# Kernel optimization log

Measured on AMD Instinct MI355X. Metric: run time of the kernel, lower is better.

The kernel has to match this reference:

```python
import jax, jax.numpy as jnp
import numpy as np

N1, N2, K = 262144, 65536, 16   # dense points, coarse points, knn neighbors
CIN, COUT = 64, 64              # in_planes, out_planes
EPS = 1e-5


def bn(x, g, b, m, v):
    # eval-mode BatchNorm1d with learned affine and running stats
    return (x - m) * jax.lax.rsqrt(v + EPS) * g + b


def setup_inputs() -> dict:
    key = jax.random.key(0)
    ks = jax.random.split(key, 32)
    u = lambda k, *s: jax.random.normal(k, s, jnp.float32)
    lin = lambda k, o, i: jax.random.normal(k, (o, i), jnp.float32) / np.float32(np.sqrt(i))
    inp = dict(
        p1=u(ks[0], N1, 3), p2=u(ks[1], N2, 3),
        x1=u(ks[2], N1, COUT), x2=u(ks[3], N2, CIN),
        knn_idx=jax.random.randint(ks[4], (N2, K), 0, N1),
        # linear1: Linear(COUT,COUT) + BN + ReLU
        w1=lin(ks[5], COUT, COUT), b1=0.01 * u(ks[6], COUT),
        g1=jnp.ones(COUT), be1=jnp.zeros(COUT),
        m1=0.1 * u(ks[7], COUT), v1=jax.random.uniform(ks[8], (COUT,), minval=0.5, maxval=1.5),
        # linear2: Linear(CIN,COUT) + BN + ReLU
        w2=lin(ks[9], COUT, CIN), b2=0.01 * u(ks[10], COUT),
        g2=jnp.ones(COUT), be2=jnp.zeros(COUT),
        m2=0.1 * u(ks[11], COUT), v2=jax.random.uniform(ks[12], (COUT,), minval=0.5, maxval=1.5),
        # channel_shrinker: Linear(CIN+3,CIN) + BN + ReLU + Linear(CIN,1)
        ws1=lin(ks[13], CIN, CIN + 3), bs1=0.01 * u(ks[14], CIN),
        gs=jnp.ones(CIN), bes=jnp.zeros(CIN),
        ms=0.1 * u(ks[15], CIN), vs=jax.random.uniform(ks[16], (CIN,), minval=0.5, maxval=1.5),
        ws2=lin(ks[17], 1, CIN), bs2=0.01 * u(ks[18], 1),
    )
    return inp


def reference(p1, p2, x1, x2, knn_idx,
              w1, b1, g1, be1, m1, v1,
              w2, b2, g2, be2, m2, v2,
              ws1, bs1, gs, bes, ms, vs, ws2, bs2):
    idx = knn_idx.reshape(-1)                                   # [M] = [N2*K], indices into p1
    # relative position of each knn neighbor to its coarse query point
    p_r = p1[idx].reshape(N2, K, 3) - p2[:, None, :]            # [N2,K,3]
    x2k = jnp.concatenate(
        [p_r, jnp.broadcast_to(x2[:, None, :], (N2, K, CIN))], axis=-1
    ).reshape(N2 * K, CIN + 3)                                  # [M, CIN+3]
    # channel_shrinker MLP -> scalar logit per (coarse, neighbor) pair
    h = jax.nn.relu(bn(x2k @ ws1.T + bs1, gs, bes, ms, vs))     # [M, CIN]
    logit = (h @ ws2.T + bs2)[:, 0]                             # [M]
    # scatter_softmax over variable in-degree groups keyed by dense point idx
    gmax = jax.lax.stop_gradient(jax.ops.segment_max(logit, idx, num_segments=N1))
    e = jnp.exp(logit - gmax[idx])
    denom = jax.ops.segment_sum(e, idx, num_segments=N1)
    prob = e / denom[idx]                                       # [M]
    # linear2(x2), broadcast over K neighbors, weight, scatter-sum to dense points
    up_feat = jax.nn.relu(bn(x2 @ w2.T + b2, g2, be2, m2, v2))  # [N2, COUT]
    weighted = (up_feat[:, None, :] * prob.reshape(N2, K, 1)).reshape(N2 * K, COUT)
    up = jax.ops.segment_sum(weighted, idx, num_segments=N1)    # [N1, COUT]
    # skip branch: linear1(x1)
    y1 = jax.nn.relu(bn(x1 @ w1.T + b1, g1, be1, m1, v1))       # [N1, COUT]
    return y1 + up
```

## Files before the change

### kernel.cpp

```cpp
#include <hip/hip_runtime.h>

#define CN1 262144
#define CN2 65536
#define CK  16
#define CM  (CN2*CK)

typedef unsigned short u16;
typedef unsigned char  u8;
typedef unsigned int   u32;
typedef float f32x4 __attribute__((ext_vector_type(4)));

__device__ __forceinline__ float b2f(u16 h) {
    union { u32 u; float f; } v; v.u = ((u32)h) << 16; return v.f;
}
__device__ __forceinline__ u16 f2b(float f) {
    union { float f; u32 u; } v; v.f = f;
    u32 lsb = (v.u >> 16) & 1u;
    return (u16)((v.u + 0x7FFFu + lsb) >> 16);
}
__device__ __forceinline__ float u2f(u32 u) {
    union { u32 u; float f; } v; v.u = u; return v.f;
}
__device__ __forceinline__ u32 f2u(float f) {
    union { float f; u32 u; } v; v.f = f; return v.u;
}

#define W_POS   0
#define W_FT    256
#define W_AS    12544
#define W_BS    12608
#define W_WS2   12672
#define W_A2    12736
#define W_B2    12800
#define W_A1    12864
#define W_B1    12928
#define W_BS2   12992
#define W_MODE  13000
#define W_W1T   13056
#define W_W2T   17152
#define W_JP    21248

__device__ __forceinline__ float ldv(const void* p, size_t i, int bf) {
    return bf ? b2f(((const u16*)p)[i]) : ((const float*)p)[i];
}

#define FMA4(A, Wv) \
    (A).x = fmaf(xv_, (Wv).x, (A).x); (A).y = fmaf(xv_, (Wv).y, (A).y); \
    (A).z = fmaf(xv_, (Wv).z, (A).z); (A).w = fmaf(xv_, (Wv).w, (A).w);

#define DECL_ACC16 \
    f32x4 A0={0,0,0,0},A1={0,0,0,0},A2={0,0,0,0},A3={0,0,0,0}, \
          A4={0,0,0,0},A5={0,0,0,0},A6={0,0,0,0},A7={0,0,0,0}, \
          A8={0,0,0,0},A9={0,0,0,0},A10={0,0,0,0},A11={0,0,0,0}, \
          A12={0,0,0,0},A13={0,0,0,0},A14={0,0,0,0},A15={0,0,0,0};

#define WSTEP16(wt, ivar, xval) { \
    float xv_ = (xval); \
    const f32x4* wr_ = (const f32x4*)((wt) + ((size_t)(ivar) << 6)); \
    FMA4(A0, wr_[0])   FMA4(A1, wr_[1])   FMA4(A2, wr_[2])   FMA4(A3, wr_[3]) \
    FMA4(A4, wr_[4])   FMA4(A5, wr_[5])   FMA4(A6, wr_[6])   FMA4(A7, wr_[7]) \
    FMA4(A8, wr_[8])   FMA4(A9, wr_[9])   FMA4(A10,wr_[10])  FMA4(A11,wr_[11]) \
    FMA4(A12,wr_[12])  FMA4(A13,wr_[13])  FMA4(A14,wr_[14])  FMA4(A15,wr_[15]) }

#define GEMV64T(bf, xrow_f, xrow_u4, wt) \
    if (bf) { \
        const uint4* xu_ = (xrow_u4); \
        _Pragma("unroll 2") \
        for (int ii_ = 0; ii_ < 8; ++ii_) { \
            uint4 xc_ = xu_[ii_]; \
            WSTEP16(wt, ii_*8+0, b2f((u16)(xc_.x & 0xffffu))) \
            WSTEP16(wt, ii_*8+1, b2f((u16)(xc_.x >> 16))) \
            WSTEP16(wt, ii_*8+2, b2f((u16)(xc_.y & 0xffffu))) \
            WSTEP16(wt, ii_*8+3, b2f((u16)(xc_.y >> 16))) \
            WSTEP16(wt, ii_*8+4, b2f((u16)(xc_.z & 0xffffu))) \
            WSTEP16(wt, ii_*8+5, b2f((u16)(xc_.z >> 16))) \
            WSTEP16(wt, ii_*8+6, b2f((u16)(xc_.w & 0xffffu))) \
            WSTEP16(wt, ii_*8+7, b2f((u16)(xc_.w >> 16))) \
        } \
    } else { \
        const float4* xf_ = (xrow_f); \
        _Pragma("unroll 2") \
        for (int ii_ = 0; ii_ < 8; ++ii_) { \
            float4 xa_ = xf_[2*ii_], xb_ = xf_[2*ii_+1]; \
            WSTEP16(wt, ii_*8+0, xa_.x) WSTEP16(wt, ii_*8+1, xa_.y) \
            WSTEP16(wt, ii_*8+2, xa_.z) WSTEP16(wt, ii_*8+3, xa_.w) \
            WSTEP16(wt, ii_*8+4, xb_.x) WSTEP16(wt, ii_*8+5, xb_.y) \
            WSTEP16(wt, ii_*8+6, xb_.z) WSTEP16(wt, ii_*8+7, xb_.w) \
        } \
    }

#define DECL_ACC8 \
    f32x4 A0={0,0,0,0},A1={0,0,0,0},A2={0,0,0,0},A3={0,0,0,0}, \
          A4={0,0,0,0},A5={0,0,0,0},A6={0,0,0,0},A7={0,0,0,0};

#define WSTEP8(wtco, ivar, xval) { \
    float xv_ = (xval); \
    const f32x4* wr_ = (const f32x4*)((wtco) + ((size_t)(ivar) << 6)); \
    FMA4(A0, wr_[0])  FMA4(A1, wr_[1])  FMA4(A2, wr_[2])  FMA4(A3, wr_[3]) \
    FMA4(A4, wr_[4])  FMA4(A5, wr_[5])  FMA4(A6, wr_[6])  FMA4(A7, wr_[7]) }

#define GEMV32T(bf, xrow_f, xrow_u4, wtco) \
    if (bf) { \
        const uint4* xu_ = (xrow_u4); \
        _Pragma("unroll 2") \
        for (int ii_ = 0; ii_ < 8; ++ii_) { \
            uint4 xc_ = xu_[ii_]; \
            WSTEP8(wtco, ii_*8+0, b2f((u16)(xc_.x & 0xffffu))) \
            WSTEP8(wtco, ii_*8+1, b2f((u16)(xc_.x >> 16))) \
            WSTEP8(wtco, ii_*8+2, b2f((u16)(xc_.y & 0xffffu))) \
            WSTEP8(wtco, ii_*8+3, b2f((u16)(xc_.y >> 16))) \
            WSTEP8(wtco, ii_*8+4, b2f((u16)(xc_.z & 0xffffu))) \
            WSTEP8(wtco, ii_*8+5, b2f((u16)(xc_.z >> 16))) \
            WSTEP8(wtco, ii_*8+6, b2f((u16)(xc_.w & 0xffffu))) \
            WSTEP8(wtco, ii_*8+7, b2f((u16)(xc_.w >> 16))) \
        } \
    } else { \
        const float4* xf_ = (xrow_f); \
        _Pragma("unroll 2") \
        for (int ii_ = 0; ii_ < 8; ++ii_) { \
            float4 xa_ = xf_[2*ii_], xb_ = xf_[2*ii_+1]; \
            WSTEP8(wtco, ii_*8+0, xa_.x) WSTEP8(wtco, ii_*8+1, xa_.y) \
            WSTEP8(wtco, ii_*8+2, xa_.z) WSTEP8(wtco, ii_*8+3, xa_.w) \
            WSTEP8(wtco, ii_*8+4, xb_.x) WSTEP8(wtco, ii_*8+5, xb_.y) \
            WSTEP8(wtco, ii_*8+6, xb_.z) WSTEP8(wtco, ii_*8+7, xb_.w) \
        } \
    }

#define BNR1(A, av, bv) \
    (A).x = fmaxf(fmaf((A).x,(av).x,(bv).x),0.f); \
    (A).y = fmaxf(fmaf((A).y,(av).y,(bv).y),0.f); \
    (A).z = fmaxf(fmaf((A).z,(av).z,(bv).z),0.f); \
    (A).w = fmaxf(fmaf((A).w,(av).w,(bv).w),0.f);
#define BNR16(aBase, bBase) { \
    const f32x4* av_ = (const f32x4*)(aBase); \
    const f32x4* bv_ = (const f32x4*)(bBase); \
    BNR1(A0,av_[0],bv_[0])   BNR1(A1,av_[1],bv_[1]) \
    BNR1(A2,av_[2],bv_[2])   BNR1(A3,av_[3],bv_[3]) \
    BNR1(A4,av_[4],bv_[4])   BNR1(A5,av_[5],bv_[5]) \
    BNR1(A6,av_[6],bv_[6])   BNR1(A7,av_[7],bv_[7]) \
    BNR1(A8,av_[8],bv_[8])   BNR1(A9,av_[9],bv_[9]) \
    BNR1(A10,av_[10],bv_[10]) BNR1(A11,av_[11],bv_[11]) \
    BNR1(A12,av_[12],bv_[12]) BNR1(A13,av_[13],bv_[13]) \
    BNR1(A14,av_[14],bv_[14]) BNR1(A15,av_[15],bv_[15]) }
#define BNR8(aBase, bBase) { \
    const f32x4* av_ = (const f32x4*)(aBase); \
    const f32x4* bv_ = (const f32x4*)(bBase); \
    BNR1(A0,av_[0],bv_[0]) BNR1(A1,av_[1],bv_[1]) \
    BNR1(A2,av_[2],bv_[2]) BNR1(A3,av_[3],bv_[3]) \
    BNR1(A4,av_[4],bv_[4]) BNR1(A5,av_[5],bv_[5]) \
    BNR1(A6,av_[6],bv_[6]) BNR1(A7,av_[7],bv_[7]) }

#define UFQ(q, AL, AH) { uint4 u_ = ufr_[q]; \
    (AL).x = fmaf(pe_, b2f((u16)(u_.x & 0xffffu)), (AL).x); \
    (AL).y = fmaf(pe_, b2f((u16)(u_.x >> 16)),     (AL).y); \
    (AL).z = fmaf(pe_, b2f((u16)(u_.y & 0xffffu)), (AL).z); \
    (AL).w = fmaf(pe_, b2f((u16)(u_.y >> 16)),     (AL).w); \
    (AH).x = fmaf(pe_, b2f((u16)(u_.z & 0xffffu)), (AH).x); \
    (AH).y = fmaf(pe_, b2f((u16)(u_.z >> 16)),     (AH).y); \
    (AH).z = fmaf(pe_, b2f((u16)(u_.w & 0xffffu)), (AH).z); \
    (AH).w = fmaf(pe_, b2f((u16)(u_.w >> 16)),     (AH).w); }

#define STQ(q, AL, AH, dst) { uint4 o_; \
    o_.x = (u32)f2b((AL).x) | ((u32)f2b((AL).y) << 16); \
    o_.y = (u32)f2b((AL).z) | ((u32)f2b((AL).w) << 16); \
    o_.z = (u32)f2b((AH).x) | ((u32)f2b((AH).y) << 16); \
    o_.w = (u32)f2b((AH).z) | ((u32)f2b((AH).w) << 16); \
    ((uint4*)(dst))[q] = o_; }
#define STORE_BF16V(dst) \
    STQ(0,A0,A1,dst)  STQ(1,A2,A3,dst)  STQ(2,A4,A5,dst)  STQ(3,A6,A7,dst) \
    STQ(4,A8,A9,dst)  STQ(5,A10,A11,dst) STQ(6,A12,A13,dst) STQ(7,A14,A15,dst)
#define STORE_F3216(dst) { f32x4* ov_ = (f32x4*)(dst); \
    ov_[0]=A0;  ov_[1]=A1;  ov_[2]=A2;  ov_[3]=A3; \
    ov_[4]=A4;  ov_[5]=A5;  ov_[6]=A6;  ov_[7]=A7; \
    ov_[8]=A8;  ov_[9]=A9;  ov_[10]=A10;ov_[11]=A11; \
    ov_[12]=A12;ov_[13]=A13;ov_[14]=A14;ov_[15]=A15; }
#define STORE_BF8V(dst) \
    STQ(0,A0,A1,dst) STQ(1,A2,A3,dst) STQ(2,A4,A5,dst) STQ(3,A6,A7,dst)
#define STORE_F328(dst) { f32x4* ov_ = (f32x4*)(dst); \
    ov_[0]=A0; ov_[1]=A1; ov_[2]=A2; ov_[3]=A3; \
    ov_[4]=A4; ov_[5]=A5; ov_[6]=A6; ov_[7]=A7; }

__global__ __launch_bounds__(256) void k_prep(
    const void* __restrict__ w1,  const void* __restrict__ b1,  const void* __restrict__ g1,
    const void* __restrict__ be1, const void* __restrict__ m1,  const void* __restrict__ v1,
    const void* __restrict__ w2,  const void* __restrict__ b2,  const void* __restrict__ g2,
    const void* __restrict__ be2, const void* __restrict__ m2,  const void* __restrict__ v2,
    const void* __restrict__ ws1, const void* __restrict__ bs1, const void* __restrict__ gs,
    const void* __restrict__ bes, const void* __restrict__ ms,  const void* __restrict__ vs,
    const void* __restrict__ ws2, const void* __restrict__ bs2, float* __restrict__ wb,
    u32* __restrict__ offsets, u32* __restrict__ cursor)
{
    int b = blockIdx.x;
    int tid = threadIdx.x;
    if (b > 0) {
        offsets[(b - 1) * 256 + tid] = 0u;
        if (b == 1 && tid == 0) *cursor = 0u;
        return;
    }

    u32 w0 = ((const u32*)g1)[0];
    int bf = (w0 != 0x3F800000u) ? 1 : 0;

    for (int t = tid; t < 64*64; t += 256) {
        int i = t >> 6, c = t & 63;
        wb[W_FT  + t] = ldv(ws1, (size_t)c*67 + 3 + i, bf);
        wb[W_W1T + t] = ldv(w1,  (size_t)c*64 + i, bf);
        wb[W_W2T + t] = ldv(w2,  (size_t)c*64 + i, bf);
    }
    for (int t = tid; t < 64*3; t += 256) {
        int j = t / 3, k = t % 3;
        wb[W_POS + t] = ldv(ws1, (size_t)j*67 + k, bf);
    }
    if (tid < 64) {
        float as = ldv(gs, tid, bf) * rsqrtf(ldv(vs, tid, bf) + 1e-5f);
        float bs = (ldv(bs1, tid, bf) - ldv(ms, tid, bf)) * as + ldv(bes, tid, bf);
        float wc = ldv(ws2, tid, bf);
        wb[W_AS + tid] = as;
        wb[W_BS + tid] = bs;
        wb[W_WS2 + tid] = wc;
        float a2 = ldv(g2, tid, bf) * rsqrtf(ldv(v2, tid, bf) + 1e-5f);
        wb[W_A2 + tid] = a2;
        wb[W_B2 + tid] = (ldv(b2, tid, bf) - ldv(m2, tid, bf)) * a2 + ldv(be2, tid, bf);
        float a1 = ldv(g1, tid, bf) * rsqrtf(ldv(v1, tid, bf) + 1e-5f);
        wb[W_A1 + tid] = a1;
        wb[W_B1 + tid] = (ldv(b1, tid, bf) - ldv(m1, tid, bf)) * a1 + ldv(be1, tid, bf);
        wb[W_JP + tid*8 + 0] = ldv(ws1, (size_t)tid*67 + 0, bf);
        wb[W_JP + tid*8 + 1] = ldv(ws1, (size_t)tid*67 + 1, bf);
        wb[W_JP + tid*8 + 2] = ldv(ws1, (size_t)tid*67 + 2, bf);
        wb[W_JP + tid*8 + 3] = as;
        wb[W_JP + tid*8 + 4] = bs;
        wb[W_JP + tid*8 + 5] = wc;
        wb[W_JP + tid*8 + 6] = 0.f;
        wb[W_JP + tid*8 + 7] = 0.f;
    }
    if (tid == 0) {
        wb[W_BS2] = ldv(bs2, 0, bf);
        ((u32*)wb)[W_MODE] = (u32)bf;
    }
}

__global__ __launch_bounds__(256, 8) void k_coarse2(
    const void* __restrict__ x2, const int* __restrict__ knn,
    const float* __restrict__ wb,
    float* __restrict__ dots, u16* __restrict__ upfeat,
    u32* __restrict__ offsets, u8* __restrict__ rank8)
{
    int bf   = (int)((const u32*)wb)[W_MODE];
    int tid  = threadIdx.x;
    int role = blockIdx.x & 1;
    int lane = tid & 63;
    int co   = __builtin_amdgcn_readfirstlane(((tid >> 6) & 1) << 5);
    int n2   = (blockIdx.x >> 1) * 128 + (tid >> 7) * 64 + lane;
    const float4* xf = (const float4*)((const float*)x2 + (size_t)n2 * 64);
    const uint4*  xu = (const uint4*)((const u16*)x2 + (size_t)n2 * 64);

    if (role == 0) {
        if (co == 0) {
            const int4* kv = (const int4*)(knn + (size_t)n2 * 16);
            u32 rw0, rw1, rw2, rw3;
            #define CNT4(T, RW) { \
                u32 r0_ = atomicAdd(&offsets[(T).x & (CN1-1)], 1u); \
                u32 r1_ = atomicAdd(&offsets[(T).y & (CN1-1)], 1u); \
                u32 r2_ = atomicAdd(&offsets[(T).z & (CN1-1)], 1u); \
                u32 r3_ = atomicAdd(&offsets[(T).w & (CN1-1)], 1u); \
                RW = (r0_ & 0xffu) | ((r1_ & 0xffu) << 8) | \
                     ((r2_ & 0xffu) << 16) | ((r3_ & 0xffu) << 24); }
            int4 t0 = kv[0]; CNT4(t0, rw0)
            int4 t1 = kv[1]; CNT4(t1, rw1)
            int4 t2 = kv[2]; CNT4(t2, rw2)
            int4 t3 = kv[3]; CNT4(t3, rw3)
            #undef CNT4
            uint4 rv; rv.x = rw0; rv.y = rw1; rv.z = rw2; rv.w = rw3;
            ((uint4*)rank8)[n2] = rv;
        }
        DECL_ACC8
        GEMV32T(bf, xf, xu, wb + W_FT + co)
        STORE_F328(dots + (size_t)n2 * 64 + co)
    } else {
        DECL_ACC8
        GEMV32T(bf, xf, xu, wb + W_W2T + co)
        BNR8(wb + W_A2 + co, wb + W_B2 + co)
        STORE_BF8V(upfeat + (size_t)n2 * 64 + co)
    }
}

__global__ __launch_bounds__(256) void k_scan(
    u32* __restrict__ offsets, u32* __restrict__ cursor)
{
    __shared__ u32 s[256];
    __shared__ u32 base;
    int t = threadIdx.x;
    int i = blockIdx.x * 256 + t;
    u32 v = offsets[i];
    s[t] = v; __syncthreads();
    for (int off = 1; off < 256; off <<= 1) {
        u32 add = (t >= off) ? s[t-off] : 0u;
        __syncthreads();
        s[t] += add;
        __syncthreads();
    }
    u32 inc = s[t];
    if (t == 255) base = atomicAdd(cursor, inc);
    __syncthreads();
    offsets[i] = ((base + inc - v) << 6) | (v & 63u);
}

#define LSTEP4(j, dv, LG) { f32x4 pa_ = jp[2*(j)], pb_ = jp[2*(j)+1]; \
    float pre_ = fmaf(prz, pa_.z, fmaf(pry, pa_.y, fmaf(prx, pa_.x, (dv)))); \
    float h_ = fmaxf(fmaf(pre_, pa_.w, pb_.x), 0.f); \
    LG = fmaf(h_, pb_.y, LG); }

__global__ __launch_bounds__(256) void k_logit_scatter(
    const void* __restrict__ p1, const void* __restrict__ p2,
    const int* __restrict__ knn, const float* __restrict__ wb,
    const float* __restrict__ dots, const u8* __restrict__ rank8,
    const u32* __restrict__ offsets, uint2* __restrict__ epair)
{
    int bf = (int)((const u32*)wb)[W_MODE];
    int m  = blockIdx.x * 256 + threadIdx.x;
    int n2 = m >> 4;

    int idx = knn[m] & (CN1-1);
    u32 rk  = (u32)rank8[m];
    u32 pos = ((offsets[idx] >> 6) + rk) & (CM-1);

    float prx = ldv(p1, (size_t)idx*3+0, bf) - ldv(p2, (size_t)n2*3+0, bf);
    float pry = ldv(p1, (size_t)idx*3+1, bf) - ldv(p2, (size_t)n2*3+1, bf);
    float prz = ldv(p1, (size_t)idx*3+2, bf) - ldv(p2, (size_t)n2*3+2, bf);

    const f32x4*  jp  = (const f32x4*)(wb + W_JP);
    const float4* dr4 = (const float4*)(dots + (size_t)n2 * 64);
    float lg0 = 0.f, lg1 = 0.f, lg2 = 0.f, lg3 = 0.f;
    #pragma unroll 4
    for (int jq = 0; jq < 16; ++jq) {
        float4 d4 = dr4[jq];
        LSTEP4(jq*4+0, d4.x, lg0) LSTEP4(jq*4+1, d4.y, lg1)
        LSTEP4(jq*4+2, d4.z, lg2) LSTEP4(jq*4+3, d4.w, lg3)
    }
    uint2 e;
    e.x = (u32)m;
    e.y = f2u(((lg0 + lg1) + (lg2 + lg3)) + wb[W_BS2]);
    epair[pos] = e;
}

__global__ __launch_bounds__(256, 4) void k_dense(
    const void* __restrict__ x1, const float* __restrict__ wb,
    const uint2* __restrict__ epair, const u16* __restrict__ upfeat,
    const u32* __restrict__ offsets, void* __restrict__ out)
{
    int bf = (int)((const u32*)wb)[W_MODE];
    int n1 = blockIdx.x * 256 + threadIdx.x;

    u32 pk = offsets[n1];
    int d = (int)(pk & 63u);
    int start = (int)(pk >> 6);

    float mxv = -3.0e38f, s = 0.f;
    for (int e = 0; e < d; ++e) {
        float l = u2f(epair[(u32)(start + e) & (CM-1)].y);
        float mnew = fmaxf(mxv, l);
        s = fmaf(s, __expf(mxv - mnew), __expf(l - mnew));
        mxv = mnew;
    }
    float inv = (d > 0) ? (1.f / s) : 0.f;

    DECL_ACC16
    GEMV64T(bf, (const float4*)((const float*)x1 + (size_t)n1 * 64),
                (const uint4*)((const u16*)x1 + (size_t)n1 * 64),
                wb + W_W1T)
    BNR16(wb + W_A1, wb + W_B1)

    for (int e = 0; e < d; ++e) {
        uint2 t = epair[(u32)(start + e) & (CM-1)];
        float pe_ = __expf(u2f(t.y) - mxv) * inv;
        u32 m = t.x & (CM-1);
        const uint4* ufr_ = (const uint4*)(upfeat + (size_t)(m >> 4) * 64);
        UFQ(0,A0,A1)   UFQ(1,A2,A3)   UFQ(2,A4,A5)   UFQ(3,A6,A7)
        UFQ(4,A8,A9)   UFQ(5,A10,A11) UFQ(6,A12,A13) UFQ(7,A14,A15)
    }

    if (bf) { u16* orow = (u16*)out + (size_t)n1 * 64; STORE_BF16V(orow) }
    else    { STORE_F3216((float*)out + (size_t)n1 * 64) }
}

extern "C" void kernel_launch(void* const* d_in, const int* in_sizes, int n_in,
                              void* d_out, int out_size, void* d_ws, size_t ws_size,
                              hipStream_t stream)
{
    (void)in_sizes; (void)n_in; (void)out_size; (void)ws_size;
    const void* p1   = d_in[0];
    const void* p2   = d_in[1];
    const void* x1   = d_in[2];
    const void* x2   = d_in[3];
    const int*  knn  = (const int*)d_in[4];
    const void* w1   = d_in[5];
    const void* b1   = d_in[6];
    const void* g1   = d_in[7];
    const void* be1  = d_in[8];
    const void* m1   = d_in[9];
    const void* v1   = d_in[10];
    const void* w2   = d_in[11];
    const void* b2   = d_in[12];
    const void* g2   = d_in[13];
    const void* be2  = d_in[14];
    const void* m2   = d_in[15];
    const void* v2   = d_in[16];
    const void* ws1  = d_in[17];
    const void* bs1  = d_in[18];
    const void* gs   = d_in[19];
    const void* bes  = d_in[20];
    const void* ms   = d_in[21];
    const void* vs   = d_in[22];
    const void* ws2w = d_in[23];
    const void* bs2  = d_in[24];

    char* ws = (char*)d_ws;
    float* wb      = (float*)(ws);
    uint2* epair   = (uint2*)(ws + ((size_t)1  << 20));
    u16*   upfeat  = (u16*)  (ws + ((size_t)9  << 20));
    u32*   offsets = (u32*)  (ws + ((size_t)17 << 20));
    u32*   cursor  = (u32*)  (ws + ((size_t)18 << 20));
    u8*    rank8   = (u8*)   (ws + ((size_t)19 << 20));
    float* dots    = (float*)d_out;

    k_prep          <<<1 + CN1/256, 256, 0, stream>>>(w1,b1,g1,be1,m1,v1,
                                                      w2,b2,g2,be2,m2,v2,
                                                      ws1,bs1,gs,bes,ms,vs,
                                                      ws2w, bs2, wb, offsets, cursor);
    k_coarse2       <<<2*(CN2/128), 256, 0, stream>>>(x2, knn, wb, dots, upfeat,
                                                      offsets, rank8);
    k_scan          <<<CN1/256,     256, 0, stream>>>(offsets, cursor);
    k_logit_scatter <<<CM/256,      256, 0, stream>>>(p1, p2, knn, wb, dots,
                                                      rank8, offsets, epair);
    k_dense         <<<CN1/256,     256, 0, stream>>>(x1, wb, epair, upfeat,
                                                      offsets, d_out);
}
```

Before: 195.6 us.

## Store projected dots in bf16, split knn counting across wavefronts, prefetch epair

The per-coarse-point projection 'dots' is now stored as bf16 instead of fp32, halving the intermediate write in k_coarse2 and the read in k_logit_scatter, which unpacks the values in registers. The atomic in-degree counting in k_coarse2 is spread over both wavefront halves, each handling 8 of the 16 neighbors, instead of being done only by the co==0 half. k_dense software-prefetches the next epair entry while it accumulates the current one. Storing dots in bf16 adds rounding error to the logits.

```diff
diff --git a/kernel.cpp b/kernel.cpp
--- a/kernel.cpp
+++ b/kernel.cpp
@@ -242,7 +242,7 @@
 __global__ __launch_bounds__(256, 8) void k_coarse2(
     const void* __restrict__ x2, const int* __restrict__ knn,
     const float* __restrict__ wb,
-    float* __restrict__ dots, u16* __restrict__ upfeat,
+    u16* __restrict__ dots, u16* __restrict__ upfeat,
     u32* __restrict__ offsets, u8* __restrict__ rank8)
 {
     int bf   = (int)((const u32*)wb)[W_MODE];
@@ -255,27 +255,25 @@
     const uint4*  xu = (const uint4*)((const u16*)x2 + (size_t)n2 * 64);
 
     if (role == 0) {
-        if (co == 0) {
-            const int4* kv = (const int4*)(knn + (size_t)n2 * 16);
-            u32 rw0, rw1, rw2, rw3;
-            #define CNT4(T, RW) { \
-                u32 r0_ = atomicAdd(&offsets[(T).x & (CN1-1)], 1u); \
-                u32 r1_ = atomicAdd(&offsets[(T).y & (CN1-1)], 1u); \
-                u32 r2_ = atomicAdd(&offsets[(T).z & (CN1-1)], 1u); \
-                u32 r3_ = atomicAdd(&offsets[(T).w & (CN1-1)], 1u); \
-                RW = (r0_ & 0xffu) | ((r1_ & 0xffu) << 8) | \
-                     ((r2_ & 0xffu) << 16) | ((r3_ & 0xffu) << 24); }
-            int4 t0 = kv[0]; CNT4(t0, rw0)
-            int4 t1 = kv[1]; CNT4(t1, rw1)
-            int4 t2 = kv[2]; CNT4(t2, rw2)
-            int4 t3 = kv[3]; CNT4(t3, rw3)
-            #undef CNT4
-            uint4 rv; rv.x = rw0; rv.y = rw1; rv.z = rw2; rv.w = rw3;
-            ((uint4*)rank8)[n2] = rv;
-        }
+        int half = co >> 5;
+        const int4* kv = (const int4*)(knn + (size_t)n2 * 16);
+        u32 rwA, rwB;
+        #define CNT4(T, RW) { \
+            u32 r0_ = atomicAdd(&offsets[(T).x & (CN1-1)], 1u); \
+            u32 r1_ = atomicAdd(&offsets[(T).y & (CN1-1)], 1u); \
+            u32 r2_ = atomicAdd(&offsets[(T).z & (CN1-1)], 1u); \
+            u32 r3_ = atomicAdd(&offsets[(T).w & (CN1-1)], 1u); \
+            RW = (r0_ & 0xffu) | ((r1_ & 0xffu) << 8) | \
+                 ((r2_ & 0xffu) << 16) | ((r3_ & 0xffu) << 24); }
+        int4 tA = kv[half*2 + 0]; CNT4(tA, rwA)
+        int4 tB = kv[half*2 + 1]; CNT4(tB, rwB)
+        #undef CNT4
+        uint2 rv2; rv2.x = rwA; rv2.y = rwB;
+        ((uint2*)rank8)[(size_t)n2*2 + half] = rv2;
+
         DECL_ACC8
         GEMV32T(bf, xf, xu, wb + W_FT + co)
-        STORE_F328(dots + (size_t)n2 * 64 + co)
+        STORE_BF8V(dots + (size_t)n2 * 64 + co)
     } else {
         DECL_ACC8
         GEMV32T(bf, xf, xu, wb + W_W2T + co)
@@ -313,7 +311,7 @@
 __global__ __launch_bounds__(256) void k_logit_scatter(
     const void* __restrict__ p1, const void* __restrict__ p2,
     const int* __restrict__ knn, const float* __restrict__ wb,
-    const float* __restrict__ dots, const u8* __restrict__ rank8,
+    const u16* __restrict__ dots, const u8* __restrict__ rank8,
     const u32* __restrict__ offsets, uint2* __restrict__ epair)
 {
     int bf = (int)((const u32*)wb)[W_MODE];
@@ -328,14 +326,20 @@
     float pry = ldv(p1, (size_t)idx*3+1, bf) - ldv(p2, (size_t)n2*3+1, bf);
     float prz = ldv(p1, (size_t)idx*3+2, bf) - ldv(p2, (size_t)n2*3+2, bf);
 
-    const f32x4*  jp  = (const f32x4*)(wb + W_JP);
-    const float4* dr4 = (const float4*)(dots + (size_t)n2 * 64);
+    const f32x4* jp  = (const f32x4*)(wb + W_JP);
+    const uint4* dr8 = (const uint4*)(dots + (size_t)n2 * 64);
     float lg0 = 0.f, lg1 = 0.f, lg2 = 0.f, lg3 = 0.f;
-    #pragma unroll 4
-    for (int jq = 0; jq < 16; ++jq) {
-        float4 d4 = dr4[jq];
-        LSTEP4(jq*4+0, d4.x, lg0) LSTEP4(jq*4+1, d4.y, lg1)
-        LSTEP4(jq*4+2, d4.z, lg2) LSTEP4(jq*4+3, d4.w, lg3)
+    #pragma unroll 2
+    for (int jq = 0; jq < 8; ++jq) {
+        uint4 dv = dr8[jq];
+        LSTEP4(jq*8+0, b2f((u16)(dv.x & 0xffffu)), lg0)
+        LSTEP4(jq*8+1, b2f((u16)(dv.x >> 16)),     lg1)
+        LSTEP4(jq*8+2, b2f((u16)(dv.y & 0xffffu)), lg2)
+        LSTEP4(jq*8+3, b2f((u16)(dv.y >> 16)),     lg3)
+        LSTEP4(jq*8+4, b2f((u16)(dv.z & 0xffffu)), lg0)
+        LSTEP4(jq*8+5, b2f((u16)(dv.z >> 16)),     lg1)
+        LSTEP4(jq*8+6, b2f((u16)(dv.w & 0xffffu)), lg2)
+        LSTEP4(jq*8+7, b2f((u16)(dv.w >> 16)),     lg3)
     }
     uint2 e;
     e.x = (u32)m;
@@ -370,13 +374,15 @@
                 wb + W_W1T)
     BNR16(wb + W_A1, wb + W_B1)
 
+    uint2 tc = epair[(u32)start & (CM-1)];
     for (int e = 0; e < d; ++e) {
-        uint2 t = epair[(u32)(start + e) & (CM-1)];
-        float pe_ = __expf(u2f(t.y) - mxv) * inv;
-        u32 m = t.x & (CM-1);
+        uint2 tn = epair[(u32)(start + e + 1) & (CM-1)];
+        float pe_ = __expf(u2f(tc.y) - mxv) * inv;
+        u32 m = tc.x & (CM-1);
         const uint4* ufr_ = (const uint4*)(upfeat + (size_t)(m >> 4) * 64);
         UFQ(0,A0,A1)   UFQ(1,A2,A3)   UFQ(2,A4,A5)   UFQ(3,A6,A7)
         UFQ(4,A8,A9)   UFQ(5,A10,A11) UFQ(6,A12,A13) UFQ(7,A14,A15)
+        tc = tn;
     }
 
     if (bf) { u16* orow = (u16*)out + (size_t)n1 * 64; STORE_BF16V(orow) }
@@ -421,7 +427,7 @@
     u32*   offsets = (u32*)  (ws + ((size_t)17 << 20));
     u32*   cursor  = (u32*)  (ws + ((size_t)18 << 20));
     u8*    rank8   = (u8*)   (ws + ((size_t)19 << 20));
-    float* dots    = (float*)d_out;
+    u16*   dots    = (u16*)d_out;
 
     k_prep          <<<1 + CN1/256, 256, 0, stream>>>(w1,b1,g1,be1,m1,v1,
                                                       w2,b2,g2,be2,m2,v2,
```

After: 192.8 us. Within noise of the previous version (-1.4%).
